# Optimization experiments

Hardware: AMD Instinct MI355X
Metric: run time of the kernel (lower is better)

Reference implementation:

```python
import jax, jax.numpy as jnp
import numpy as np

D_MODEL = 1024
N_HEADS = 16
N_PHASE = 128
HEAD_DIM = D_MODEL // N_HEADS
PHASE_PER_HEAD = N_PHASE // N_HEADS
CONTENT_SCALE = 1.0 / np.sqrt(HEAD_DIM)
PHASE_SCALE = 1.0 / np.sqrt(PHASE_PER_HEAD)
LN_EPS = 1e-5


def create_position_phases(L, n_phase, base=10000.0):
    # RoPE-style: each freq repeated at even/odd indices (interleaved)
    inv_freq = 1.0 / base ** (jnp.arange(0, n_phase, 2, dtype=jnp.float32) / n_phase)
    pos = jnp.arange(L, dtype=jnp.float32)
    sinusoid = pos[:, None] * inv_freq[None, :]          # (L, n_phase//2)
    return jnp.repeat(sinusoid, 2, axis=1)               # (L, n_phase)


def setup_inputs() -> dict:
    key = jax.random.key(0)
    ks = jax.random.split(key, 12)
    B, L, D, P = 1, 2048, D_MODEL, N_PHASE
    s = 0.02
    return {
        'x_real': jax.random.normal(ks[0], (B, L, D), jnp.float32),
        'x_imag': jax.random.normal(ks[1], (B, L, D), jnp.float32),
        'Wq': jax.random.normal(ks[2], (D, D), jnp.float32) * s,
        'Wk': jax.random.normal(ks[3], (D, D), jnp.float32) * s,
        'Wv': jax.random.normal(ks[4], (D, D), jnp.float32) * s,
        'Wqp': jax.random.normal(ks[5], (D, P), jnp.float32) * s,
        'bqp': jax.random.uniform(ks[6], (P,), jnp.float32, -np.pi, np.pi),
        'Wkp': jax.random.normal(ks[7], (D, P), jnp.float32) * s,
        'bkp': jax.random.uniform(ks[8], (P,), jnp.float32, -np.pi, np.pi),
        'Wo': jax.random.normal(ks[9], (D, D), jnp.float32) * s,
        'alpha_logit': jnp.zeros((N_HEADS, 1, 1), jnp.float32),
        'ln_gamma': jnp.ones((D,), jnp.float32),
        'ln_beta': jnp.zeros((D,), jnp.float32),
    }


def _split_heads(x, B, L, H, hd):
    return x.reshape(B, L, H, hd).transpose(0, 2, 1, 3)  # (B,H,L,hd)


def reference(x_real, x_imag, Wq, Wk, Wv, Wqp, bqp, Wkp, bkp, Wo,
              alpha_logit, ln_gamma, ln_beta):
    B, L, D = x_real.shape
    H, hd, p = N_HEADS, HEAD_DIM, PHASE_PER_HEAD

    Q = _split_heads(x_real @ Wq, B, L, H, hd)
    K = _split_heads(x_real @ Wk, B, L, H, hd)
    V = _split_heads(x_real @ Wv, B, L, H, hd)
    content = jnp.einsum('bhqd,bhkd->bhqk', Q, K) * CONTENT_SCALE

    pos_phase = create_position_phases(L, N_PHASE)        # (L, P)
    Qt = _split_heads(x_imag @ Wqp + bqp + pos_phase, B, L, H, p)
    Kt = _split_heads(x_imag @ Wkp + bkp + pos_phase, B, L, H, p)
    phase = (jnp.einsum('bhqp,bhkp->bhqk', jnp.cos(Qt), jnp.cos(Kt))
             + jnp.einsum('bhqp,bhkp->bhqk', jnp.sin(Qt), jnp.sin(Kt))) * PHASE_SCALE

    alpha = jax.nn.sigmoid(alpha_logit)                   # (H,1,1) broadcasts over (B,H,L,L)
    scores = (1.0 - alpha) * content + alpha * phase

    causal = jnp.triu(jnp.ones((L, L), bool), 1)
    scores = jnp.where(causal, -jnp.inf, scores)
    attn = jax.nn.softmax(scores, axis=-1)

    out = jnp.einsum('bhqk,bhkd->bhqd', attn, V)
    out = out.transpose(0, 2, 1, 3).reshape(B, L, D) @ Wo

    h = x_real + out
    mu = jnp.mean(h, axis=-1, keepdims=True)
    var = jnp.var(h, axis=-1, keepdims=True)
    out_real = (h - mu) / jnp.sqrt(var + LN_EPS) * ln_gamma + ln_beta
    return out_real, x_imag
```

## Files before the change

### kernel.cpp

```cpp
#include <hip/hip_runtime.h>
#include <hip/hip_bf16.h>
#include <math.h>

#define L 2048
#define D 1024
#define NH 16
#define HD 64
#define P 128
#define HDE 96
#define CONTENT_SCALE 0.125f
#define PHASE_SCALE   0.35355339059327373f
#define KLS 104
#define VT2 136
#define NSPLIT 2

typedef short bf16x8 __attribute__((ext_vector_type(8)));
typedef float f32x4 __attribute__((ext_vector_type(4)));
typedef float f32x16 __attribute__((ext_vector_type(16)));

__device__ inline ushort f2b(float x) {
    __hip_bfloat16 b = __float2bfloat16(x);
    return *(ushort*)&b;
}
__device__ inline float b2f(ushort u) {
    unsigned v = (unsigned)u << 16;
    union { unsigned u; float f; } c; c.u = v; return c.f;
}

__device__ inline void sincos_hw(float ang, float* sn, float* cs) {
    float rev = ang * 0.15915494309189535f;
    rev -= floorf(rev);
    *sn = __builtin_amdgcn_sinf(rev);
    *cs = __builtin_amdgcn_cosf(rev);
}

__device__ inline void gld_lds16(const void* g, void* l) {
    __builtin_amdgcn_global_load_lds(
        (const __attribute__((address_space(1))) unsigned int*)g,
        (__attribute__((address_space(3))) unsigned int*)l,
        16, 0, 0);
}

__global__ void prep_kernel(const float* __restrict__ xr, const float* __restrict__ xi,
                            ushort* __restrict__ xrb, ushort* __restrict__ xib,
                            const float* __restrict__ W0, const float* __restrict__ W1,
                            const float* __restrict__ W2, const float* __restrict__ W3,
                            const float* __restrict__ W4, const float* __restrict__ W5,
                            ushort* __restrict__ T0, ushort* __restrict__ T1,
                            ushort* __restrict__ T2, ushort* __restrict__ T3,
                            ushort* __restrict__ Tp,
                            ushort* __restrict__ Qe, ushort* __restrict__ Ke) {
    __shared__ float tile[32][33];
    const int b = blockIdx.x;
    const int tid = threadIdx.x;
    if (b < 4096) {
        const float4* src = (b >> 11) ? (const float4*)xi : (const float4*)xr;
        ushort4* dst = (b >> 11) ? (ushort4*)xib : (ushort4*)xrb;
        int i = ((b & 2047) << 8) + tid;
        float4 v = src[i];
        ushort4 o;
        o.x = f2b(v.x); o.y = f2b(v.y); o.z = f2b(v.z); o.w = f2b(v.w);
        dst[i] = o;
    } else if (b < 8448) {
        int w = b - 4096;
        const float* W; ushort* T; int ncols, n0, k0;
        if (w < 4096) {
            int z = w >> 10, t = w & 1023;
            n0 = (t & 31) * 32; k0 = (t >> 5) * 32; ncols = D;
            W = (z == 0) ? W0 : ((z == 1) ? W1 : ((z == 2) ? W2 : W3));
            T = (z == 0) ? T0 : ((z == 1) ? T1 : ((z == 2) ? T2 : T3));
        } else {
            int w2 = w - 4096;
            int z = w2 >> 7, t = w2 & 127;
            n0 = (t & 3) * 32; k0 = (t >> 2) * 32; ncols = P;
            W = z ? W5 : W4;
            T = Tp + (size_t)z * P * D;
        }
        int tx = tid & 31, ty = tid >> 5;
#pragma unroll
        for (int i = 0; i < 4; i++)
            tile[ty + i * 8][tx] = W[(size_t)(k0 + ty + i * 8) * ncols + n0 + tx];
        __syncthreads();
#pragma unroll
        for (int i = 0; i < 4; i++)
            T[(size_t)(n0 + ty + i * 8) * D + k0 + tx] = f2b(tile[tx][ty + i * 8]);
    } else {
        int i = (b - 8448) * 256 + tid;
        size_t base = (size_t)i * HDE + 80;
        uint4 z4 = make_uint4(0, 0, 0, 0);
        *(uint4*)(Qe + base) = z4;
        *(uint4*)(Qe + base + 8) = z4;
        *(uint4*)(Ke + base) = z4;
        *(uint4*)(Ke + base + 8) = z4;
    }
}

__launch_bounds__(256)
__global__ void qkv_gemm(const ushort* __restrict__ Ab, const ushort* __restrict__ xib,
                         const ushort* __restrict__ Wtq, const ushort* __restrict__ Wtk,
                         const ushort* __restrict__ Wtv, const ushort* __restrict__ Wtp,
                         ushort* __restrict__ Qe, ushort* __restrict__ Ke,
                         ushort* __restrict__ Ve, const float* __restrict__ alpha,
                         const float* __restrict__ bqp, const float* __restrict__ bkp) {
    const int z = blockIdx.z;
    if (z == 3 && blockIdx.x >= 2) return;
    const ushort* At = (z == 3) ? xib : Ab;
    const ushort* Bt = (z == 0) ? Wtq : ((z == 1) ? Wtk : ((z == 2) ? Wtv : Wtp));
    __shared__ ushort As0[128 * 32], Bs0[128 * 32];
    __shared__ ushort As1[128 * 32], Bs1[128 * 32];
    const int tid = threadIdx.x;
    const int wave = tid >> 6, lane = tid & 63, quad = lane >> 4, ln16 = lane & 15;
    const int wm = wave >> 1, wn = wave & 1;
    const int m0 = blockIdx.y * 128, n0 = blockIdx.x * 128;
    f32x4 acc[4][4];
#pragma unroll
    for (int i = 0; i < 4; i++)
#pragma unroll
        for (int j = 0; j < 4; j++) acc[i][j] = (f32x4){0.f, 0.f, 0.f, 0.f};

    auto stage = [&](int kt, ushort* Asb, ushort* Bsb) {
#pragma unroll
        for (int i = 0; i < 2; i++) {
            int idx = i * 256 + tid;
            int r2 = idx >> 2, cc = idx & 3;
            gld_lds16(At + (size_t)(m0 + r2) * D + kt + cc * 8, &Asb[idx * 8]);
            gld_lds16(Bt + (size_t)(n0 + r2) * D + kt + cc * 8, &Bsb[idx * 8]);
        }
    };
    auto compute = [&](const ushort* Asb, const ushort* Bsb) {
        bf16x8 af[4], bfr[4];
#pragma unroll
        for (int t = 0; t < 4; t++) {
            af[t]  = *(const bf16x8*)(&Asb[(wm * 64 + t * 16 + ln16) * 32 + quad * 8]);
            bfr[t] = *(const bf16x8*)(&Bsb[(wn * 64 + t * 16 + ln16) * 32 + quad * 8]);
        }
#pragma unroll
        for (int i = 0; i < 4; i++)
#pragma unroll
            for (int j = 0; j < 4; j++)
                acc[i][j] = __builtin_amdgcn_mfma_f32_16x16x32_bf16(af[i], bfr[j], acc[i][j], 0, 0, 0);
    };

    stage(0, As0, Bs0);
    __syncthreads();
    for (int kt = 0; kt < D; kt += 64) {
        stage(kt + 32, As1, Bs1);
        compute(As0, Bs0);
        __syncthreads();
        if (kt + 64 < D) stage(kt + 64, As0, Bs0);
        compute(As1, Bs1);
        __syncthreads();
    }

    if (z == 2) {
        int hn = (n0 + wn * 64) >> 6;
#pragma unroll
        for (int i = 0; i < 4; i++)
#pragma unroll
            for (int j = 0; j < 4; j++) {
                int d = j * 16 + ln16;
                int m = m0 + wm * 64 + i * 16 + quad * 4;
                ushort4 pk;
                pk.x = f2b(acc[i][j][0]); pk.y = f2b(acc[i][j][1]);
                pk.z = f2b(acc[i][j][2]); pk.w = f2b(acc[i][j][3]);
                *(ushort4*)(Ve + ((size_t)hn * HD + d) * L + m) = pk;
            }
    } else if (z < 2) {
        int hn = (n0 + wn * 64) >> 6;
        float s = (z == 0) ? (1.f - 1.f / (1.f + __expf(-alpha[hn]))) * CONTENT_SCALE : 1.f;
        ushort* dst = (z == 0) ? Qe : Ke;
#pragma unroll
        for (int i = 0; i < 4; i++)
#pragma unroll
            for (int j = 0; j < 4; j++) {
                int dcol = j * 16 + ln16;
#pragma unroll
                for (int r = 0; r < 4; r++) {
                    int m = m0 + wm * 64 + i * 16 + quad * 4 + r;
                    dst[((size_t)hn * L + m) * HDE + dcol] = f2b(acc[i][j][r] * s);
                }
            }
    } else {
#pragma unroll
        for (int j = 0; j < 4; j++) {
            int cg = n0 + wn * 64 + j * 16 + ln16;
            int isQ = cg < P;
            int c = cg & (P - 1);
            int hh = c >> 3, jj = c & 7;
            float b = isQ ? bqp[c] : bkp[c];
            float sc = isQ ? (1.f / (1.f + __expf(-alpha[hh]))) * PHASE_SCALE : 1.f;
            float invf = __expf(-((float)(c & ~1) / 128.f) * 9.210340371976184f);
            ushort* dst = isQ ? Qe : Ke;
#pragma unroll
            for (int i = 0; i < 4; i++)
#pragma unroll
                for (int r = 0; r < 4; r++) {
                    int m = m0 + wm * 64 + i * 16 + quad * 4 + r;
                    float qt = acc[i][j][r] + b + (float)m * invf;
                    float sn, cs;
                    sincos_hw(qt, &sn, &cs);
                    size_t base = ((size_t)hh * L + m) * HDE;
                    dst[base + 64 + jj] = f2b(sc * cs);
                    dst[base + 72 + jj] = f2b(sc * sn);
                }
        }
    }
}

__launch_bounds__(256, 2)
__global__ void flash_attn(const ushort* __restrict__ Qe, const ushort* __restrict__ Ke,
                           const ushort* __restrict__ Vte,
                           ushort* __restrict__ Opart, float* __restrict__ ml) {
    const int b = blockIdx.x;
    const int xcd = b & 7;
    const int r = b >> 3;
    const int idx = r & 31, sub = r >> 5;
    const int hbit = idx >> 4, c0i = idx & 15;
    const int c = sub ? 15 - c0i : c0i;
    const int z = sub;
    const int h = xcd * 2 + hbit;
    const int tid = threadIdx.x;
    const int wave = tid >> 6, lane = tid & 63;
    const int ln32 = lane & 31, hf = lane >> 5;

    const int nT = c + 1;
    const int s0 = z * nT;
    const int nR = (nT + 1) >> 1;
    const int qw = c * 128 + wave * 32;

    __shared__ ushort Kl[128 * KLS];
    __shared__ ushort Vt[64 * VT2];

    const ushort* Kh = Ke + (size_t)h * L * HDE;
    const ushort* Vh = Vte + (size_t)h * HD * L;
    const ushort* Qh = Qe + (size_t)h * L * HDE;
    ushort* Op = Opart + (size_t)z * L * D;
    float* mlp = ml + (size_t)z * NH * L + (size_t)h * L;

    bf16x8 onesv;
#pragma unroll
    for (int i = 0; i < 8; i++) onesv[i] = (short)0x3F80;

    bf16x8 qa[6];
#pragma unroll
    for (int cc = 0; cc < 6; cc++)
        qa[cc] = *(const bf16x8*)(Qh + (size_t)(qw + ln32) * HDE + cc * 16 + hf * 8);

    f32x16 o[2], olv;
#pragma unroll
    for (int i = 0; i < 16; i++) { o[0][i] = 0.f; o[1][i] = 0.f; olv[i] = 0.f; }

    int rowk[6], colk[6];
#pragma unroll
    for (int ii = 0; ii < 6; ii++) {
        int ix = ii * 256 + tid;
        rowk[ii] = ix / 12; colk[ii] = ix - rowk[ii] * 12;
    }
    int dv[4], cv[4];
#pragma unroll
    for (int ii = 0; ii < 4; ii++) {
        int ix = ii * 256 + tid;
        dv[ii] = ix >> 4; cv[ii] = ix & 15;
    }

    bf16x8 kreg[6], vreg[4];
    {
        int kk = s0 * 64;
#pragma unroll
        for (int ii = 0; ii < 6; ii++)
            kreg[ii] = *(const bf16x8*)(Kh + (size_t)(kk + rowk[ii]) * HDE + colk[ii] * 8);
#pragma unroll
        for (int ii = 0; ii < 4; ii++)
            vreg[ii] = *(const bf16x8*)(Vh + (size_t)dv[ii] * L + kk + cv[ii] * 8);
    }

    for (int rr = 0; rr < nR; rr++) {
        const int tk0 = (s0 + rr * 2) * 64;
        __syncthreads();
#pragma unroll
        for (int ii = 0; ii < 6; ii++)
            *(bf16x8*)(&Kl[rowk[ii] * KLS + colk[ii] * 8]) = kreg[ii];
#pragma unroll
        for (int ii = 0; ii < 4; ii++)
            *(bf16x8*)(&Vt[dv[ii] * VT2 + cv[ii] * 8]) = vreg[ii];
        __syncthreads();

        if (rr + 1 < nR) {
            int kk = tk0 + 128;
#pragma unroll
            for (int ii = 0; ii < 6; ii++)
                kreg[ii] = *(const bf16x8*)(Kh + (size_t)(kk + rowk[ii]) * HDE + colk[ii] * 8);
#pragma unroll
            for (int ii = 0; ii < 4; ii++)
                vreg[ii] = *(const bf16x8*)(Vh + (size_t)dv[ii] * L + kk + cv[ii] * 8);
        }

#pragma unroll
        for (int hb = 0; hb < 2; hb++) {
            const int tt = rr * 2 + hb;
            const int k0 = tk0 + hb * 64;
            if (tt < nT && k0 < qw + 32) {
                f32x16 s2[2];
#pragma unroll
                for (int i = 0; i < 16; i++) { s2[0][i] = 0.f; s2[1][i] = 0.f; }
                __builtin_amdgcn_s_setprio(1);
#pragma unroll
                for (int kb = 0; kb < 2; kb++)
#pragma unroll
                    for (int cc = 0; cc < 6; cc++) {
                        bf16x8 kf = *(const bf16x8*)(&Kl[(hb * 64 + kb * 32 + ln32) * KLS + cc * 16 + hf * 8]);
                        s2[kb] = __builtin_amdgcn_mfma_f32_32x32x16_bf16(kf, qa[cc], s2[kb], 0, 0, 0);
                    }
                __builtin_amdgcn_s_setprio(0);

                if (k0 + 63 > qw) {
#pragma unroll
                    for (int kb = 0; kb < 2; kb++)
#pragma unroll
                        for (int rg = 0; rg < 16; rg++) {
                            int key = k0 + kb * 32 + (rg & 3) + 8 * (rg >> 2) + 4 * hf;
                            if (key > qw + ln32) s2[kb][rg] = -1e30f;
                        }
                }

#pragma unroll
                for (int kb = 0; kb < 2; kb++)
#pragma unroll
                    for (int rg = 0; rg < 16; rg++)
                        s2[kb][rg] = __expf(s2[kb][rg]);

                unsigned Xp[2][4], Yp[2][4];
#pragma unroll
                for (int kb = 0; kb < 2; kb++)
#pragma unroll
                    for (int tq = 0; tq < 4; tq++) {
                        asm("v_cvt_pk_bf16_f32 %0, %1, %2"
                            : "=v"(Xp[kb][tq]) : "v"(s2[kb][4 * tq + 0]), "v"(s2[kb][4 * tq + 1]));
                        asm("v_cvt_pk_bf16_f32 %0, %1, %2"
                            : "=v"(Yp[kb][tq]) : "v"(s2[kb][4 * tq + 2]), "v"(s2[kb][4 * tq + 3]));
                    }

                bf16x8 pa[4];
#pragma unroll
                for (int m = 0; m < 4; m++) {
                    int kb = m >> 1, te = 2 * (m & 1), to = te + 1;
                    unsigned x0 = Xp[kb][te], x1 = Xp[kb][to];
                    unsigned y0 = Yp[kb][te], y1 = Yp[kb][to];
                    asm("v_permlane32_swap_b32 %0, %1" : "+v"(x0), "+v"(x1));
                    asm("v_permlane32_swap_b32 %0, %1" : "+v"(y0), "+v"(y1));
                    union { unsigned u[4]; bf16x8 v; } pb;
                    pb.u[0] = x0; pb.u[1] = y0; pb.u[2] = x1; pb.u[3] = y1;
                    pa[m] = pb.v;
                }

                __builtin_amdgcn_s_setprio(1);
#pragma unroll
                for (int m = 0; m < 4; m++) {
#pragma unroll
                    for (int db = 0; db < 2; db++) {
                        bf16x8 vf = *(const bf16x8*)(&Vt[(db * 32 + ln32) * VT2 + hb * 64 + m * 16 + hf * 8]);
                        o[db] = __builtin_amdgcn_mfma_f32_32x32x16_bf16(pa[m], vf, o[db], 0, 0, 0);
                    }
                    olv = __builtin_amdgcn_mfma_f32_32x32x16_bf16(pa[m], onesv, olv, 0, 0, 0);
                }
                __builtin_amdgcn_s_setprio(0);
            }
        }
    }

    if (ln32 == 0) {
#pragma unroll
        for (int rg = 0; rg < 16; rg++) {
            int q = qw + (rg & 3) + 8 * (rg >> 2) + 4 * hf;
            mlp[q] = olv[rg];
        }
    }
#pragma unroll
    for (int db = 0; db < 2; db++)
#pragma unroll
        for (int rg = 0; rg < 16; rg++) {
            int q = qw + (rg & 3) + 8 * (rg >> 2) + 4 * hf;
            Op[(size_t)q * D + h * HD + db * 32 + ln32] = f2b(o[db][rg]);
        }
}

__global__ void comb_kernel(const ushort* __restrict__ Opart, const float* __restrict__ ml,
                            ushort* __restrict__ AOb) {
    int q = blockIdx.x;
    int t = threadIdx.x;
    int h = t >> 4;
    float lsum = 0.f;
#pragma unroll
    for (int zz = 0; zz < NSPLIT; zz++)
        lsum += ml[(size_t)zz * NH * L + (size_t)h * L + q];
    float inv = 1.f / lsum;
    size_t idx = (size_t)q * D + t * 4;
    float ox = 0.f, oy = 0.f, oz = 0.f, ow = 0.f;
#pragma unroll
    for (int zz = 0; zz < NSPLIT; zz++) {
        ushort4 a = *(const ushort4*)(Opart + (size_t)zz * L * D + idx);
        ox += b2f(a.x); oy += b2f(a.y); oz += b2f(a.z); ow += b2f(a.w);
    }
    ushort4 o;
    o.x = f2b(ox * inv); o.y = f2b(oy * inv);
    o.z = f2b(oz * inv); o.w = f2b(ow * inv);
    *(ushort4*)(AOb + idx) = o;
}

__launch_bounds__(256)
__global__ void wo_gemm(const ushort* __restrict__ Ab, const ushort* __restrict__ Bt,
                        float* __restrict__ C) {
    __shared__ ushort As0[128 * 32], Bs0[128 * 32];
    __shared__ ushort As1[128 * 32], Bs1[128 * 32];
    const int tid = threadIdx.x;
    const int wave = tid >> 6, lane = tid & 63, quad = lane >> 4, ln16 = lane & 15;
    const int wm = wave >> 1, wn = wave & 1;
    const int m0 = blockIdx.y * 128, n0 = blockIdx.x * 128;
    f32x4 acc[4][4];
#pragma unroll
    for (int i = 0; i < 4; i++)
#pragma unroll
        for (int j = 0; j < 4; j++) acc[i][j] = (f32x4){0.f, 0.f, 0.f, 0.f};

    auto stage = [&](int kt, ushort* Asb, ushort* Bsb) {
#pragma unroll
        for (int i = 0; i < 2; i++) {
            int idx = i * 256 + tid;
            int r2 = idx >> 2, cc = idx & 3;
            gld_lds16(Ab + (size_t)(m0 + r2) * D + kt + cc * 8, &Asb[idx * 8]);
            gld_lds16(Bt + (size_t)(n0 + r2) * D + kt + cc * 8, &Bsb[idx * 8]);
        }
    };
    auto compute = [&](const ushort* Asb, const ushort* Bsb) {
        bf16x8 af[4], bfr[4];
#pragma unroll
        for (int t = 0; t < 4; t++) {
            af[t]  = *(const bf16x8*)(&Asb[(wm * 64 + t * 16 + ln16) * 32 + quad * 8]);
            bfr[t] = *(const bf16x8*)(&Bsb[(wn * 64 + t * 16 + ln16) * 32 + quad * 8]);
        }
#pragma unroll
        for (int i = 0; i < 4; i++)
#pragma unroll
            for (int j = 0; j < 4; j++)
                acc[i][j] = __builtin_amdgcn_mfma_f32_16x16x32_bf16(af[i], bfr[j], acc[i][j], 0, 0, 0);
    };

    stage(0, As0, Bs0);
    __syncthreads();
    for (int kt = 0; kt < D; kt += 64) {
        stage(kt + 32, As1, Bs1);
        compute(As0, Bs0);
        __syncthreads();
        if (kt + 64 < D) stage(kt + 64, As0, Bs0);
        compute(As1, Bs1);
        __syncthreads();
    }
#pragma unroll
    for (int i = 0; i < 4; i++)
#pragma unroll
        for (int j = 0; j < 4; j++)
#pragma unroll
            for (int r = 0; r < 4; r++) {
                int m = m0 + wm * 64 + i * 16 + quad * 4 + r;
                int n = n0 + wn * 64 + j * 16 + ln16;
                C[(size_t)m * D + n] = acc[i][j][r];
            }
}

__global__ void ln_kernel(const float* __restrict__ xr, const float* __restrict__ o2,
                          const float* __restrict__ gamma, const float* __restrict__ beta,
                          float* __restrict__ outp, const float4* __restrict__ xi4,
                          float4* __restrict__ out1) {
    int l = blockIdx.x;
    int tid = threadIdx.x;
    int wave = tid >> 6;
    __shared__ float red[8];
    float hv[4];
    float s = 0.f;
#pragma unroll
    for (int i = 0; i < 4; i++) {
        int c = tid + i * 256;
        hv[i] = xr[(size_t)l * D + c] + o2[(size_t)l * D + c];
        s += hv[i];
    }
    out1[(size_t)l * (D / 4) + tid] = xi4[(size_t)l * (D / 4) + tid];
#pragma unroll
    for (int off = 1; off < 64; off <<= 1) s += __shfl_xor(s, off);
    if ((tid & 63) == 0) red[wave] = s;
    __syncthreads();
    float mu = (red[0] + red[1] + red[2] + red[3]) * (1.f / D);
    float v = 0.f;
#pragma unroll
    for (int i = 0; i < 4; i++) { float d = hv[i] - mu; v += d * d; }
#pragma unroll
    for (int off = 1; off < 64; off <<= 1) v += __shfl_xor(v, off);
    __syncthreads();
    if ((tid & 63) == 0) red[4 + wave] = v;
    __syncthreads();
    float rstd = rsqrtf((red[4] + red[5] + red[6] + red[7]) * (1.f / D) + 1e-5f);
#pragma unroll
    for (int i = 0; i < 4; i++) {
        int c = tid + i * 256;
        outp[(size_t)l * D + c] = (hv[i] - mu) * rstd * gamma[c] + beta[c];
    }
}

extern "C" void kernel_launch(void* const* d_in, const int* in_sizes, int n_in,
                              void* d_out, int out_size, void* d_ws, size_t ws_size,
                              hipStream_t stream) {
    const float* xr    = (const float*)d_in[0];
    const float* xi    = (const float*)d_in[1];
    const float* Wq    = (const float*)d_in[2];
    const float* Wk    = (const float*)d_in[3];
    const float* Wv    = (const float*)d_in[4];
    const float* Wqp   = (const float*)d_in[5];
    const float* bqp   = (const float*)d_in[6];
    const float* Wkp   = (const float*)d_in[7];
    const float* bkp   = (const float*)d_in[8];
    const float* Wo    = (const float*)d_in[9];
    const float* alpha = (const float*)d_in[10];
    const float* gamma = (const float*)d_in[11];
    const float* beta  = (const float*)d_in[12];

    const size_t LD = (size_t)L * D;
    const size_t MB = 1024 * 1024;

    char* A8 = (char*)d_out;
    char* B8 = A8 + LD * 4;
    ushort* xib = (ushort*)A8;
    ushort* AOb = (ushort*)A8;
    ushort* Wot = (ushort*)(A8 + 4 * MB);
    ushort* Wtq = (ushort*)(A8 + 6 * MB);
    ushort* xrb = (ushort*)B8;
    ushort* Wtk = (ushort*)(B8 + 4 * MB);
    ushort* Wtv = (ushort*)(B8 + 6 * MB);
    float* outf = (float*)d_out;

    ushort* Qe = (ushort*)d_ws;
    ushort* Ke = Qe + (size_t)NH * L * HDE;
    ushort* Ve = Ke + (size_t)NH * L * HDE;
    ushort* Wqpkt = Ve + (size_t)NH * L * HD;
    ushort* Opart = Wqpkt + (size_t)256 * D;
    float*  mlbuf = (float*)(Opart + (size_t)NSPLIT * LD);
    float*  O2 = (float*)d_ws;

    prep_kernel<<<8576, 256, 0, stream>>>(xr, xi, xrb, xib,
                                          Wq, Wk, Wv, Wo, Wqp, Wkp,
                                          Wtq, Wtk, Wtv, Wot, Wqpkt, Qe, Ke);

    qkv_gemm<<<dim3(8, 16, 4), 256, 0, stream>>>(xrb, xib, Wtq, Wtk, Wtv, Wqpkt,
                                                 Qe, Ke, Ve, alpha, bqp, bkp);

    flash_attn<<<512, 256, 0, stream>>>(Qe, Ke, Ve, Opart, mlbuf);

    comb_kernel<<<L, 256, 0, stream>>>(Opart, mlbuf, AOb);

    wo_gemm<<<dim3(8, 16), 256, 0, stream>>>(AOb, Wot, O2);

    ln_kernel<<<L, 256, 0, stream>>>(xr, O2, gamma, beta, outf,
                                     (const float4*)xi, (float4*)(B8));
}
```

Measured before the change: 182.8 us.

## Fuse split-attention combine into Wo GEMM A-operand load

Drops the separate combine kernel. The Wo GEMM now reads both bf16 partial attention outputs directly, sums them and scales by the per-head inverse softmax denominator while staging the A tile into LDS. The output tile shrinks from 128x128 to 128x64 and the grid doubles, which gives more blocks. LDS double-buffering is replaced by register prefetch of A with a single buffer, so each K step now has two barriers. Every N-block rereads the partials and redoes the combine arithmetic, so A-side traffic and ALU work rise in exchange for one fewer launch and no intermediate round trip.

```diff
diff --git a/kernel.cpp b/kernel.cpp
--- a/kernel.cpp
+++ b/kernel.cpp
@@ -384,85 +384,85 @@
         }
 }
 
-__global__ void comb_kernel(const ushort* __restrict__ Opart, const float* __restrict__ ml,
-                            ushort* __restrict__ AOb) {
-    int q = blockIdx.x;
-    int t = threadIdx.x;
-    int h = t >> 4;
-    float lsum = 0.f;
-#pragma unroll
-    for (int zz = 0; zz < NSPLIT; zz++)
-        lsum += ml[(size_t)zz * NH * L + (size_t)h * L + q];
-    float inv = 1.f / lsum;
-    size_t idx = (size_t)q * D + t * 4;
-    float ox = 0.f, oy = 0.f, oz = 0.f, ow = 0.f;
-#pragma unroll
-    for (int zz = 0; zz < NSPLIT; zz++) {
-        ushort4 a = *(const ushort4*)(Opart + (size_t)zz * L * D + idx);
-        ox += b2f(a.x); oy += b2f(a.y); oz += b2f(a.z); ow += b2f(a.w);
-    }
-    ushort4 o;
-    o.x = f2b(ox * inv); o.y = f2b(oy * inv);
-    o.z = f2b(oz * inv); o.w = f2b(ow * inv);
-    *(ushort4*)(AOb + idx) = o;
-}
-
 __launch_bounds__(256)
-__global__ void wo_gemm(const ushort* __restrict__ Ab, const ushort* __restrict__ Bt,
-                        float* __restrict__ C) {
-    __shared__ ushort As0[128 * 32], Bs0[128 * 32];
-    __shared__ ushort As1[128 * 32], Bs1[128 * 32];
+__global__ void wo_gemm(const ushort* __restrict__ Opart, const float* __restrict__ ml,
+                        const ushort* __restrict__ Bt, float* __restrict__ C) {
+    __shared__ ushort As[128 * 32];
+    __shared__ ushort Bs[64 * 32];
+    __shared__ float linv[128 * 16];
     const int tid = threadIdx.x;
     const int wave = tid >> 6, lane = tid & 63, quad = lane >> 4, ln16 = lane & 15;
-    const int wm = wave >> 1, wn = wave & 1;
-    const int m0 = blockIdx.y * 128, n0 = blockIdx.x * 128;
-    f32x4 acc[4][4];
-#pragma unroll
-    for (int i = 0; i < 4; i++)
+    const int m0 = blockIdx.y * 128, n0 = blockIdx.x * 64;
+    const size_t LD = (size_t)L * D;
+
+#pragma unroll
+    for (int i = 0; i < 8; i++) {
+        int ix = i * 256 + tid;
+        int rr = ix >> 4, hh = ix & 15;
+        float l0 = ml[(size_t)hh * L + m0 + rr];
+        float l1 = ml[(size_t)NH * L + (size_t)hh * L + m0 + rr];
+        linv[ix] = 1.f / (l0 + l1);
+    }
+
+    const int arow = tid >> 1, ac = (tid & 1) * 16;
+    const int brow = tid >> 2, bc8 = tid & 3;
+
+    f32x4 acc[2][4];
+#pragma unroll
+    for (int i = 0; i < 2; i++)
 #pragma unroll
         for (int j = 0; j < 4; j++) acc[i][j] = (f32x4){0.f, 0.f, 0.f, 0.f};
 
-    auto stage = [&](int kt, ushort* Asb, ushort* Bsb) {
-#pragma unroll
-        for (int i = 0; i < 2; i++) {
-            int idx = i * 256 + tid;
-            int r2 = idx >> 2, cc = idx & 3;
-            gld_lds16(Ab + (size_t)(m0 + r2) * D + kt + cc * 8, &Asb[idx * 8]);
-            gld_lds16(Bt + (size_t)(n0 + r2) * D + kt + cc * 8, &Bsb[idx * 8]);
-        }
-    };
-    auto compute = [&](const ushort* Asb, const ushort* Bsb) {
-        bf16x8 af[4], bfr[4];
-#pragma unroll
-        for (int t = 0; t < 4; t++) {
-            af[t]  = *(const bf16x8*)(&Asb[(wm * 64 + t * 16 + ln16) * 32 + quad * 8]);
-            bfr[t] = *(const bf16x8*)(&Bsb[(wn * 64 + t * 16 + ln16) * 32 + quad * 8]);
-        }
-#pragma unroll
-        for (int i = 0; i < 4; i++)
+    bf16x8 a0v0, a0v1, a1v0, a1v1;
+    {
+        const ushort* a0 = Opart + (size_t)(m0 + arow) * D + ac;
+        a0v0 = *(const bf16x8*)(a0);      a0v1 = *(const bf16x8*)(a0 + 8);
+        a1v0 = *(const bf16x8*)(a0 + LD); a1v1 = *(const bf16x8*)(a0 + LD + 8);
+    }
+
+    for (int kt = 0; kt < D; kt += 32) {
+        __syncthreads();
+        {
+            float iv = linv[arow * 16 + ((kt + ac) >> 6)];
+            bf16x8 w0, w1;
+#pragma unroll
+            for (int j = 0; j < 8; j++) {
+                w0[j] = (short)f2b((b2f((ushort)a0v0[j]) + b2f((ushort)a1v0[j])) * iv);
+                w1[j] = (short)f2b((b2f((ushort)a0v1[j]) + b2f((ushort)a1v1[j])) * iv);
+            }
+            *(bf16x8*)(&As[arow * 32 + ac]) = w0;
+            *(bf16x8*)(&As[arow * 32 + ac + 8]) = w1;
+        }
+        gld_lds16(Bt + (size_t)(n0 + brow) * D + kt + bc8 * 8, &Bs[tid * 8]);
+        __syncthreads();
+
+        if (kt + 32 < D) {
+            const ushort* a0 = Opart + (size_t)(m0 + arow) * D + kt + 32 + ac;
+            a0v0 = *(const bf16x8*)(a0);      a0v1 = *(const bf16x8*)(a0 + 8);
+            a1v0 = *(const bf16x8*)(a0 + LD); a1v1 = *(const bf16x8*)(a0 + LD + 8);
+        }
+
+        bf16x8 af[2], bfr[4];
+#pragma unroll
+        for (int i = 0; i < 2; i++)
+            af[i] = *(const bf16x8*)(&As[(wave * 32 + i * 16 + ln16) * 32 + quad * 8]);
+#pragma unroll
+        for (int j = 0; j < 4; j++)
+            bfr[j] = *(const bf16x8*)(&Bs[(j * 16 + ln16) * 32 + quad * 8]);
+#pragma unroll
+        for (int i = 0; i < 2; i++)
 #pragma unroll
             for (int j = 0; j < 4; j++)
                 acc[i][j] = __builtin_amdgcn_mfma_f32_16x16x32_bf16(af[i], bfr[j], acc[i][j], 0, 0, 0);
-    };
-
-    stage(0, As0, Bs0);
-    __syncthreads();
-    for (int kt = 0; kt < D; kt += 64) {
-        stage(kt + 32, As1, Bs1);
-        compute(As0, Bs0);
-        __syncthreads();
-        if (kt + 64 < D) stage(kt + 64, As0, Bs0);
-        compute(As1, Bs1);
-        __syncthreads();
-    }
-#pragma unroll
-    for (int i = 0; i < 4; i++)
+    }
+#pragma unroll
+    for (int i = 0; i < 2; i++)
 #pragma unroll
         for (int j = 0; j < 4; j++)
 #pragma unroll
             for (int r = 0; r < 4; r++) {
-                int m = m0 + wm * 64 + i * 16 + quad * 4 + r;
-                int n = n0 + wn * 64 + j * 16 + ln16;
+                int m = m0 + wave * 32 + i * 16 + quad * 4 + r;
+                int n = n0 + j * 16 + ln16;
                 C[(size_t)m * D + n] = acc[i][j][r];
             }
 }
@@ -528,7 +528,6 @@
     char* A8 = (char*)d_out;
     char* B8 = A8 + LD * 4;
     ushort* xib = (ushort*)A8;
-    ushort* AOb = (ushort*)A8;
     ushort* Wot = (ushort*)(A8 + 4 * MB);
     ushort* Wtq = (ushort*)(A8 + 6 * MB);
     ushort* xrb = (ushort*)B8;
@@ -553,9 +552,7 @@
 
     flash_attn<<<512, 256, 0, stream>>>(Qe, Ke, Ve, Opart, mlbuf);
 
-    comb_kernel<<<L, 256, 0, stream>>>(Opart, mlbuf, AOb);
-
-    wo_gemm<<<dim3(8, 16), 256, 0, stream>>>(AOb, Wot, O2);
+    wo_gemm<<<dim3(16, 16), 256, 0, stream>>>(Opart, mlbuf, Wot, O2);
 
     ln_kernel<<<L, 256, 0, stream>>>(xr, O2, gamma, beta, outf,
                                      (const float4*)xi, (float4*)(B8));
```

New measurement: 191.7 us. +4.9%, slower.
